# Kernel tuning notes

Hardware: AMD Instinct MI355X
Metric: run time of the kernel (lower is better)

The kernel has to match this reference:

```python
import jax, jax.numpy as jnp
import numpy as np

I, T, L, E, H, W = 256, 256, 32, 128, 7, 7
INIT_TEMPERATURE = 0.07


def setup_inputs() -> dict:
    key = jax.random.key(0)
    k1, k2, k3 = jax.random.split(key, 3)
    image_features = jax.random.normal(k1, (I, E, H, W), dtype=jnp.float32)
    text_features = jax.random.normal(k2, (T, L, E), dtype=jnp.float32)
    # valid caption lengths in [1, L] (avoid zero to prevent div-by-zero)
    text_length = jax.random.randint(k3, (T,), 1, L + 1, dtype=jnp.int32)
    logit_neg_log_temperature = jnp.asarray(-np.log(INIT_TEMPERATURE), dtype=jnp.float32)
    return {
        "image_features": image_features,
        "text_features": text_features,
        "text_length": text_length,
        "logit_neg_log_temperature": logit_neg_log_temperature,
    }


def reference(image_features, text_features, text_length, logit_neg_log_temperature):
    # image_features: [I, E, H, W]; text_features: [T, L, E]
    # per-(image, text, word) similarity over spatial positions: [I, T, L, H, W]
    match_max = jnp.einsum("iehw,tle->itlhw", image_features, text_features)
    # max over spatial dims (h, w): [I, T, L]
    match_max = jnp.max(match_max, axis=(3, 4))
    # sum over words, normalize by caption length: [I, T]
    match = jnp.sum(match_max, axis=2) / text_length.astype(match_max.dtype)
    logit_scale = jnp.exp(logit_neg_log_temperature)
    logits_per_image = match * logit_scale
    logits_per_text = match.T * logit_scale
    return (logits_per_image, logits_per_text)
```

## Files before the change

### kernel.cpp

```cpp
#include <hip/hip_runtime.h>

typedef int   v8i    __attribute__((ext_vector_type(8)));
typedef float f32x16 __attribute__((ext_vector_type(16)));

#define NI 256
#define NT 256
#define NL 32
#define NE 128
#define HW 49
#define NEG_INF (-3.0e38f)
#define SCALE1 0x7F7F7F7F


__device__ __forceinline__ unsigned char f32_to_e4m3(float f)
{
    unsigned fb = __float_as_uint(f);
    unsigned s  = (fb >> 24) & 0x80;
    int      e  = (int)((fb >> 23) & 0xFF);
    unsigned m  = fb & 0x7FFFFF;
    int ne = e - 120;
    if (ne <= 0)  return (unsigned char)s;
    if (ne > 15) { ne = 15; m = 0x600000; }
    unsigned base = ((unsigned)ne << 3) | (m >> 20);
    unsigned rem  = m & 0xFFFFF;
    if (rem > 0x80000 || (rem == 0x80000 && (base & 1))) base++;
    if (base > 0x7E) base = 0x7E;
    return (unsigned char)(s | base);
}

__global__ __launch_bounds__(256, 4)
void prep_kernel(const float* __restrict__ img,
                 const float* __restrict__ txt,
                 unsigned char* __restrict__ wsA,
                 unsigned char* __restrict__ wsB)
{
    const int tid  = threadIdx.x;
    const int wave = tid >> 6, lane = tid & 63;
    const int ml   = lane & 31, h = lane >> 5;
    const int bid  = blockIdx.x;
    if (bid < 1024) {
        int gw = bid;
        int i  = gw >> 2, mt = (gw >> 1) & 1, ks = gw & 1;
        int m  = mt * 32 + ml; if (m > HW - 1) m = HW - 1;
        int e0 = ks * 64 + h * 32 + wave * 8;
        const float* p = img + ((size_t)i * NE + e0) * HW + m;
        union { unsigned char b[8]; int2 v; } u;
        #pragma unroll
        for (int j = 0; j < 8; ++j) u.b[j] = f32_to_e4m3(p[j * HW]);
        *(int2*)(wsA + (size_t)gw * 2048 + lane * 32 + wave * 8) = u.v;
    } else {
        int bb = bid - 1024;
        int gw = bb * 2 + (wave >> 1);
        int eh = wave & 1;
        int t  = gw >> 1, ks = gw & 1;
        int e0 = ks * 64 + h * 32 + eh * 16;
        const float* p = txt + ((size_t)t * NL + ml) * NE + e0;
        union { unsigned char b[16]; int4 v; } u;
        #pragma unroll
        for (int q = 0; q < 4; ++q) {
            float4 f = *(const float4*)(p + q * 4);
            u.b[q*4+0] = f32_to_e4m3(f.x); u.b[q*4+1] = f32_to_e4m3(f.y);
            u.b[q*4+2] = f32_to_e4m3(f.z); u.b[q*4+3] = f32_to_e4m3(f.w);
        }
        *(int4*)(wsB + (size_t)gw * 2048 + lane * 32 + eh * 16) = u.v;
    }
}

__global__ __launch_bounds__(256, 4)
void clip_match_kernel(const unsigned char* __restrict__ wsA,
                       const unsigned char* __restrict__ wsB,
                       const int* __restrict__ tlen,
                       const float* __restrict__ nlt,
                       float* __restrict__ out)
{
    const int tid  = threadIdx.x;
    const int wave = tid >> 6, lane = tid & 63;
    const int ml   = lane & 31, h = lane >> 5;
    const int tb   = blockIdx.x & 15;
    const int ig   = blockIdx.x >> 4;
    const int im   = ig * 4 + wave;

    __shared__ __align__(16) float colmax[4][16][68];

    const unsigned char* pa = wsA + (size_t)im * 8192 + lane * 32;
    v8i aA0 = *(const v8i*)(pa);
    v8i aA1 = *(const v8i*)(pa + 2048);
    v8i aB0 = *(const v8i*)(pa + 4096);
    v8i aB1 = *(const v8i*)(pa + 6144);

    const unsigned char* csrc = wsB + (size_t)tb * 16 * 4096 + lane * 32;
#define BFR(t, k) (*(const v8i*)(csrc + (size_t)(t) * 4096 + (k) * 2048))

#define COMPUTE(bk0, bk1, t)                                                \
    {                                                                       \
        f32x16 acc0 = __builtin_amdgcn_mfma_scale_f32_32x32x64_f8f6f4(      \
            aA0, bk0, (f32x16)(0.f), 0, 0, 0, SCALE1, 0, SCALE1);           \
        acc0 = __builtin_amdgcn_mfma_scale_f32_32x32x64_f8f6f4(             \
            aA1, bk1, acc0, 0, 0, 0, SCALE1, 0, SCALE1);                    \
        f32x16 acc1 = __builtin_amdgcn_mfma_scale_f32_32x32x64_f8f6f4(      \
            aB0, bk0, (f32x16)(0.f), 0, 0, 0, SCALE1, 0, SCALE1);           \
        acc1 = __builtin_amdgcn_mfma_scale_f32_32x32x64_f8f6f4(             \
            aB1, bk1, acc1, 0, 0, 0, SCALE1, 0, SCALE1);                    \
         \
        float t0[8];                                                        \
        _Pragma("unroll")                                                   \
        for (int k = 0; k < 8; ++k) t0[k] = fmaxf(acc0[2*k], acc0[2*k+1]);  \
        float t1[4];                                                        \
        _Pragma("unroll")                                                   \
        for (int k = 0; k < 4; ++k) t1[k] = fmaxf(t0[2*k], t0[2*k+1]);      \
        float a0m = fmaxf(fmaxf(t1[0], t1[1]), fmaxf(t1[2], t1[3]));        \
        float u0[4];                                                        \
        _Pragma("unroll")                                                   \
        for (int k = 0; k < 4; ++k) u0[k] = fmaxf(acc1[2*k], acc1[2*k+1]);  \
        float a1m = fmaxf(fmaxf(u0[0], u0[1]), fmaxf(u0[2], u0[3]));        \
        float ex  = (h == 0) ? acc1[8] : NEG_INF;                           \
        colmax[wave][t][lane] = fmaxf(fmaxf(a0m, a1m), ex);                 \
    }

    v8i c0 = BFR(0, 0), c1 = BFR(0, 1);
    #pragma unroll 1
    for (int it = 0; it < 8; ++it) {
        const int t = 2 * it;
        v8i n0 = BFR(t + 1, 0), n1 = BFR(t + 1, 1);
        COMPUTE(c0, c1, t)
        if (it < 7) { c0 = BFR(t + 2, 0); c1 = BFR(t + 2, 1); }
        COMPUTE(n0, n1, t + 1)
    }
#undef COMPUTE
#undef BFR

    {
        const float scale = expf(nlt[0]);
        const int t = lane & 15;
        const int q = lane >> 4;
        const float* r0 = &colmax[wave][t][q * 8];
        const float* r1 = &colmax[wave][t][32 + q * 8];
        float4 a0 = *(const float4*)(r0 + 0);
        float4 a1 = *(const float4*)(r0 + 4);
        float4 c0 = *(const float4*)(r1 + 0);
        float4 c1 = *(const float4*)(r1 + 4);
        float s = (fmaxf(a0.x, c0.x) + fmaxf(a0.y, c0.y))
                + (fmaxf(a0.z, c0.z) + fmaxf(a0.w, c0.w))
                + (fmaxf(a1.x, c1.x) + fmaxf(a1.y, c1.y))
                + (fmaxf(a1.z, c1.z) + fmaxf(a1.w, c1.w));
        s += __shfl_xor(s, 16);
        s += __shfl_xor(s, 32);
        if (q == 0) {
            int tg = tb * 16 + t;
            float v = s * scale / (float)tlen[tg];
            out[im * NT + tg] = v;
            out[NI * NT + tg * NI + im] = v;
        }
    }
}

extern "C" void kernel_launch(void* const* d_in, const int* in_sizes, int n_in,
                              void* d_out, int out_size, void* d_ws, size_t ws_size,
                              hipStream_t stream)
{
    const float* img  = (const float*)d_in[0];
    const float* txt  = (const float*)d_in[1];
    const int*   tlen = (const int*)d_in[2];
    const float* nlt  = (const float*)d_in[3];
    float* out = (float*)d_out;

    unsigned char* wsA = (unsigned char*)d_ws;
    unsigned char* wsB = wsA + (size_t)2 * 1024 * 1024;

    prep_kernel<<<dim3(1280), dim3(256), 0, stream>>>(img, txt, wsA, wsB);
    clip_match_kernel<<<dim3(1024), dim3(256), 0, stream>>>(wsA, wsB, tlen, nlt, out);
}
```

Before: 29.14 us.

## Fuse image FP8 conversion into match kernel and double texts per block

Removes the image pre-conversion pass from the prep kernel. The match kernel now loads fp32 image features directly and converts them to e4m3 in registers before the MFMA loop. Each block now handles 32 texts instead of 16, which halves the grid and doubles the reuse of the converted A fragments. The cost is strided scalar fp32 loads and per-element conversion inside the main kernel, plus more LDS and registers per block, which is why the launch bound drops to 3 blocks.

New measurement: 71.23 us. 144% more time.

```diff
diff --git a/kernel.cpp b/kernel.cpp
--- a/kernel.cpp
+++ b/kernel.cpp
@@ -29,45 +29,31 @@
 }
 
 __global__ __launch_bounds__(256, 4)
-void prep_kernel(const float* __restrict__ img,
-                 const float* __restrict__ txt,
-                 unsigned char* __restrict__ wsA,
+void prep_kernel(const float* __restrict__ txt,
                  unsigned char* __restrict__ wsB)
 {
     const int tid  = threadIdx.x;
     const int wave = tid >> 6, lane = tid & 63;
     const int ml   = lane & 31, h = lane >> 5;
-    const int bid  = blockIdx.x;
-    if (bid < 1024) {
-        int gw = bid;
-        int i  = gw >> 2, mt = (gw >> 1) & 1, ks = gw & 1;
-        int m  = mt * 32 + ml; if (m > HW - 1) m = HW - 1;
-        int e0 = ks * 64 + h * 32 + wave * 8;
-        const float* p = img + ((size_t)i * NE + e0) * HW + m;
-        union { unsigned char b[8]; int2 v; } u;
-        #pragma unroll
-        for (int j = 0; j < 8; ++j) u.b[j] = f32_to_e4m3(p[j * HW]);
-        *(int2*)(wsA + (size_t)gw * 2048 + lane * 32 + wave * 8) = u.v;
-    } else {
-        int bb = bid - 1024;
-        int gw = bb * 2 + (wave >> 1);
-        int eh = wave & 1;
-        int t  = gw >> 1, ks = gw & 1;
-        int e0 = ks * 64 + h * 32 + eh * 16;
-        const float* p = txt + ((size_t)t * NL + ml) * NE + e0;
-        union { unsigned char b[16]; int4 v; } u;
-        #pragma unroll
-        for (int q = 0; q < 4; ++q) {
-            float4 f = *(const float4*)(p + q * 4);
-            u.b[q*4+0] = f32_to_e4m3(f.x); u.b[q*4+1] = f32_to_e4m3(f.y);
-            u.b[q*4+2] = f32_to_e4m3(f.z); u.b[q*4+3] = f32_to_e4m3(f.w);
-        }
-        *(int4*)(wsB + (size_t)gw * 2048 + lane * 32 + eh * 16) = u.v;
+    const int bb   = blockIdx.x;
+    const int t    = (bb & 7) * 32 + (bb >> 3);
+    const int ks   = wave >> 1;
+    const int eh   = wave & 1;
+    const int gw   = t * 2 + ks;
+    const int e0   = ks * 64 + h * 32 + eh * 16;
+    const float* p = txt + ((size_t)t * NL + ml) * NE + e0;
+    union { unsigned char b[16]; int4 v; } u;
+    #pragma unroll
+    for (int q = 0; q < 4; ++q) {
+        float4 f = *(const float4*)(p + q * 4);
+        u.b[q*4+0] = f32_to_e4m3(f.x); u.b[q*4+1] = f32_to_e4m3(f.y);
+        u.b[q*4+2] = f32_to_e4m3(f.z); u.b[q*4+3] = f32_to_e4m3(f.w);
     }
+    *(int4*)(wsB + (size_t)gw * 2048 + lane * 32 + eh * 16) = u.v;
 }
 
-__global__ __launch_bounds__(256, 4)
-void clip_match_kernel(const unsigned char* __restrict__ wsA,
+__global__ __launch_bounds__(256, 3)
+void clip_match_kernel(const float* __restrict__ img,
                        const unsigned char* __restrict__ wsB,
                        const int* __restrict__ tlen,
                        const float* __restrict__ nlt,
@@ -76,19 +62,33 @@
     const int tid  = threadIdx.x;
     const int wave = tid >> 6, lane = tid & 63;
     const int ml   = lane & 31, h = lane >> 5;
-    const int tb   = blockIdx.x & 15;
-    const int ig   = blockIdx.x >> 4;
+    const int tb   = blockIdx.x & 7;
+    const int ig   = blockIdx.x >> 3;
     const int im   = ig * 4 + wave;
 
-    __shared__ __align__(16) float colmax[4][16][68];
+    __shared__ __align__(16) float colmax[4][NL][68];
 
-    const unsigned char* pa = wsA + (size_t)im * 8192 + lane * 32;
-    v8i aA0 = *(const v8i*)(pa);
-    v8i aA1 = *(const v8i*)(pa + 2048);
-    v8i aB0 = *(const v8i*)(pa + 4096);
-    v8i aB1 = *(const v8i*)(pa + 6144);
+    v8i aA0, aA1, aB0, aB1;
+    {
+        const float* __restrict__ pi = img + (size_t)im * (NE * HW);
+        const int m0 = ml;
+        const int m1 = (32 + ml > HW - 1) ? HW - 1 : 32 + ml;
+        union { unsigned char b[32]; v8i v; } ua;
+        #pragma unroll
+        for (int fi = 0; fi < 4; ++fi) {
+            const int mt = fi >> 1, ks = fi & 1;
+            const int m  = mt ? m1 : m0;
+            const float* q = pi + (ks * 64 + h * 32) * HW + m;
+            #pragma unroll
+            for (int j = 0; j < 32; ++j) ua.b[j] = f32_to_e4m3(q[j * HW]);
+            if      (fi == 0) aA0 = ua.v;
+            else if (fi == 1) aA1 = ua.v;
+            else if (fi == 2) aB0 = ua.v;
+            else              aB1 = ua.v;
+        }
+    }
 
-    const unsigned char* csrc = wsB + (size_t)tb * 16 * 4096 + lane * 32;
+    const unsigned char* csrc = wsB + (size_t)tb * NL * 4096 + lane * 32;
 #define BFR(t, k) (*(const v8i*)(csrc + (size_t)(t) * 4096 + (k) * 2048))
 
 #define COMPUTE(bk0, bk1, t)                                                \
@@ -119,11 +119,11 @@
 
     v8i c0 = BFR(0, 0), c1 = BFR(0, 1);
     #pragma unroll 1
-    for (int it = 0; it < 8; ++it) {
+    for (int it = 0; it < 16; ++it) {
         const int t = 2 * it;
         v8i n0 = BFR(t + 1, 0), n1 = BFR(t + 1, 1);
         COMPUTE(c0, c1, t)
-        if (it < 7) { c0 = BFR(t + 2, 0); c1 = BFR(t + 2, 1); }
+        if (it < 15) { c0 = BFR(t + 2, 0); c1 = BFR(t + 2, 1); }
         COMPUTE(n0, n1, t + 1)
     }
 #undef COMPUTE
@@ -131,22 +131,28 @@
 
     {
         const float scale = expf(nlt[0]);
-        const int t = lane & 15;
-        const int q = lane >> 4;
-        const float* r0 = &colmax[wave][t][q * 8];
-        const float* r1 = &colmax[wave][t][32 + q * 8];
+        const int t = ml;
+        const float* r0 = &colmax[wave][t][h * 16];
+        const float* r1 = &colmax[wave][t][32 + h * 16];
         float4 a0 = *(const float4*)(r0 + 0);
         float4 a1 = *(const float4*)(r0 + 4);
+        float4 a2 = *(const float4*)(r0 + 8);
+        float4 a3 = *(const float4*)(r0 + 12);
         float4 c0 = *(const float4*)(r1 + 0);
         float4 c1 = *(const float4*)(r1 + 4);
+        float4 c2 = *(const float4*)(r1 + 8);
+        float4 c3 = *(const float4*)(r1 + 12);
         float s = (fmaxf(a0.x, c0.x) + fmaxf(a0.y, c0.y))
                 + (fmaxf(a0.z, c0.z) + fmaxf(a0.w, c0.w))
                 + (fmaxf(a1.x, c1.x) + fmaxf(a1.y, c1.y))
-                + (fmaxf(a1.z, c1.z) + fmaxf(a1.w, c1.w));
-        s += __shfl_xor(s, 16);
+                + (fmaxf(a1.z, c1.z) + fmaxf(a1.w, c1.w))
+                + (fmaxf(a2.x, c2.x) + fmaxf(a2.y, c2.y))
+                + (fmaxf(a2.z, c2.z) + fmaxf(a2.w, c2.w))
+                + (fmaxf(a3.x, c3.x) + fmaxf(a3.y, c3.y))
+                + (fmaxf(a3.z, c3.z) + fmaxf(a3.w, c3.w));
         s += __shfl_xor(s, 32);
-        if (q == 0) {
-            int tg = tb * 16 + t;
+        if (h == 0) {
+            int tg = tb * NL + t;
             float v = s * scale / (float)tlen[tg];
             out[im * NT + tg] = v;
             out[NI * NT + tg * NI + im] = v;
@@ -164,9 +170,8 @@
     const float* nlt  = (const float*)d_in[3];
     float* out = (float*)d_out;
 
-    unsigned char* wsA = (unsigned char*)d_ws;
-    unsigned char* wsB = wsA + (size_t)2 * 1024 * 1024;
+    unsigned char* wsB = (unsigned char*)d_ws;
 
-    prep_kernel<<<dim3(1280), dim3(256), 0, stream>>>(img, txt, wsA, wsB);
-    clip_match_kernel<<<dim3(1024), dim3(256), 0, stream>>>(wsA, wsB, tlen, nlt, out);
+    prep_kernel<<<dim3(256), dim3(256), 0, stream>>>(txt, wsB);
+    clip_match_kernel<<<dim3(512), dim3(256), 0, stream>>>(img, wsB, tlen, nlt, out);
 }
```

## Stage shared text tiles in LDS via global_load_lds and shuffle-reduce column max

Applied to the files above, without the earlier changes.

The text-feature fp8 tiles, which all four waves of a block use, are now loaded cooperatively into LDS with global_load_lds in two halves instead of each wave reading them straight from global memory. The prep kernel's text layout is changed to 16-byte lane chunks to match the LDS read pattern. The half-wave column max is now combined with a cross-lane shuffle before the LDS write, which shrinks the colmax buffer and the final reduction. The cost is extra LDS use (32KB per block, which may limit occupancy), block-wide barriers, and a full vmcnt wait with no overlap between loading and the MFMA work.

Result: faster. 27.40 us (median of 2 runs) (-5.9%).

```diff
diff --git a/kernel.cpp b/kernel.cpp
--- a/kernel.cpp
+++ b/kernel.cpp
@@ -62,9 +62,13 @@
             u.b[q*4+0] = f32_to_e4m3(f.x); u.b[q*4+1] = f32_to_e4m3(f.y);
             u.b[q*4+2] = f32_to_e4m3(f.z); u.b[q*4+3] = f32_to_e4m3(f.w);
         }
-        *(int4*)(wsB + (size_t)gw * 2048 + lane * 32 + eh * 16) = u.v;
+        *(int4*)(wsB + (size_t)gw * 2048 + eh * 1024 + lane * 16) = u.v;
     }
 }
+
+#define GLDS(gp, lp) __builtin_amdgcn_global_load_lds(                     \
+        (const __attribute__((address_space(1))) void*)(gp),               \
+        (__attribute__((address_space(3))) void*)(lp), 16, 0, 0)
 
 __global__ __launch_bounds__(256, 4)
 void clip_match_kernel(const unsigned char* __restrict__ wsA,
@@ -80,7 +84,8 @@
     const int ig   = blockIdx.x >> 4;
     const int im   = ig * 4 + wave;
 
-    __shared__ __align__(16) float colmax[4][16][68];
+    __shared__ __align__(16) unsigned char bstage[32768];
+    __shared__ __align__(16) float colmax[4][16][32];
 
     const unsigned char* pa = wsA + (size_t)im * 8192 + lane * 32;
     v8i aA0 = *(const v8i*)(pa);
@@ -88,8 +93,7 @@
     v8i aB0 = *(const v8i*)(pa + 4096);
     v8i aB1 = *(const v8i*)(pa + 6144);
 
-    const unsigned char* csrc = wsB + (size_t)tb * 16 * 4096 + lane * 32;
-#define BFR(t, k) (*(const v8i*)(csrc + (size_t)(t) * 4096 + (k) * 2048))
+    const unsigned char* csrc = wsB + (size_t)tb * 16 * 4096;
 
 #define COMPUTE(bk0, bk1, t)                                                \
     {                                                                       \
@@ -101,7 +105,7 @@
             aB0, bk0, (f32x16)(0.f), 0, 0, 0, SCALE1, 0, SCALE1);           \
         acc1 = __builtin_amdgcn_mfma_scale_f32_32x32x64_f8f6f4(             \
             aB1, bk1, acc1, 0, 0, 0, SCALE1, 0, SCALE1);                    \
-         \
+           \
         float t0[8];                                                        \
         _Pragma("unroll")                                                   \
         for (int k = 0; k < 8; ++k) t0[k] = fmaxf(acc0[2*k], acc0[2*k+1]);  \
@@ -114,35 +118,46 @@
         for (int k = 0; k < 4; ++k) u0[k] = fmaxf(acc1[2*k], acc1[2*k+1]);  \
         float a1m = fmaxf(fmaxf(u0[0], u0[1]), fmaxf(u0[2], u0[3]));        \
         float ex  = (h == 0) ? acc1[8] : NEG_INF;                           \
-        colmax[wave][t][lane] = fmaxf(fmaxf(a0m, a1m), ex);                 \
+        float cm  = fmaxf(fmaxf(a0m, a1m), ex);                             \
+        cm = fmaxf(cm, __shfl_xor(cm, 32));             \
+        if (h == 0) colmax[wave][t][ml] = cm;                               \
     }
 
-    v8i c0 = BFR(0, 0), c1 = BFR(0, 1);
     #pragma unroll 1
-    for (int it = 0; it < 8; ++it) {
-        const int t = 2 * it;
-        v8i n0 = BFR(t + 1, 0), n1 = BFR(t + 1, 1);
-        COMPUTE(c0, c1, t)
-        if (it < 7) { c0 = BFR(t + 2, 0); c1 = BFR(t + 2, 1); }
-        COMPUTE(n0, n1, t + 1)
+    for (int r = 0; r < 2; ++r) {
+        {
+            const unsigned char* src = csrc + r * 32768;
+            #pragma unroll
+            for (int it = 0; it < 8; ++it)
+                GLDS(src + it * 4096 + tid * 16, bstage + it * 4096 + tid * 16);
+        }
+        asm volatile("s_waitcnt vmcnt(0)" ::: "memory");
+        __builtin_amdgcn_sched_barrier(0);
+        __syncthreads();
+
+        #pragma unroll
+        for (int ts = 0; ts < 8; ++ts) {
+            const int t = r * 8 + ts;
+            union { int4 q[2]; v8i v; } b0, b1;
+            const unsigned char* base = bstage + ts * 4096 + lane * 16;
+            b0.q[0] = *(const int4*)(base);
+            b0.q[1] = *(const int4*)(base + 1024);
+            b1.q[0] = *(const int4*)(base + 2048);
+            b1.q[1] = *(const int4*)(base + 3072);
+            COMPUTE(b0.v, b1.v, t)
+        }
+        __syncthreads();
     }
-#undef COMPUTE
-#undef BFR
 
     {
         const float scale = expf(nlt[0]);
         const int t = lane & 15;
         const int q = lane >> 4;
-        const float* r0 = &colmax[wave][t][q * 8];
-        const float* r1 = &colmax[wave][t][32 + q * 8];
-        float4 a0 = *(const float4*)(r0 + 0);
-        float4 a1 = *(const float4*)(r0 + 4);
-        float4 c0 = *(const float4*)(r1 + 0);
-        float4 c1 = *(const float4*)(r1 + 4);
-        float s = (fmaxf(a0.x, c0.x) + fmaxf(a0.y, c0.y))
-                + (fmaxf(a0.z, c0.z) + fmaxf(a0.w, c0.w))
-                + (fmaxf(a1.x, c1.x) + fmaxf(a1.y, c1.y))
-                + (fmaxf(a1.z, c1.z) + fmaxf(a1.w, c1.w));
+        const float* row = &colmax[wave][t][q * 8];
+        float4 a0 = *(const float4*)(row + 0);
+        float4 a1 = *(const float4*)(row + 4);
+        float s = ((a0.x + a0.y) + (a0.z + a0.w))
+                + ((a1.x + a1.y) + (a1.z + a1.w));
         s += __shfl_xor(s, 16);
         s += __shfl_xor(s, 32);
         if (q == 0) {
```
